# Optimization experiments

Measured on AMD Instinct MI355X. Metric: run time of the kernel, lower is better.

The kernel has to match this reference:

```python
import jax, jax.numpy as jnp
import numpy as np

B, S, H, D = 2, 2048, 16, 64
HID = H * D


def setup_inputs() -> dict:
    key = jax.random.key(0)
    ks = jax.random.split(key, 9)
    s = 1.0 / np.sqrt(HID).astype(np.float32)
    return {
        "hidden_states": jax.random.normal(ks[0], (B, S, HID), dtype=jnp.float32),
        "W_q": jax.random.normal(ks[1], (HID, HID), dtype=jnp.float32) * s,
        "W_k": jax.random.normal(ks[2], (HID, HID), dtype=jnp.float32) * s,
        "W_v": jax.random.normal(ks[3], (HID, HID), dtype=jnp.float32) * s,
        "W_o": jax.random.normal(ks[4], (HID, HID), dtype=jnp.float32) * s,
        "B_q": jax.random.normal(ks[5], (HID,), dtype=jnp.float32) * 0.02,
        "B_k": jax.random.normal(ks[6], (HID,), dtype=jnp.float32) * 0.02,
        "B_v": jax.random.normal(ks[7], (HID,), dtype=jnp.float32) * 0.02,
        "B_o": jax.random.normal(ks[8], (HID,), dtype=jnp.float32) * 0.02,
    }


def _split_heads(x):
    # (B, S, H*D) -> (B, H, S, D)
    b, s, _ = x.shape
    return x.reshape(b, s, H, D).transpose(0, 2, 1, 3)


def reference(hidden_states, W_q, W_k, W_v, W_o, B_q, B_k, B_v, B_o):
    q = _split_heads(hidden_states @ W_q + B_q)
    k = _split_heads(hidden_states @ W_k + B_k)
    v = _split_heads(hidden_states @ W_v + B_v)
    scale = 1.0 / jnp.sqrt(jnp.asarray(D, dtype=q.dtype))
    # (B, H, S, S) attention scores (no mask: original forward never applies it)
    scores = jnp.einsum("bhqd,bhkd->bhqk", q, k) * scale
    weights = jax.nn.softmax(scores, axis=-1)
    attended = jnp.einsum("bhqk,bhkd->bhqd", weights, v)
    # merge heads: (B, H, S, D) -> (B, S, H*D)
    merged = attended.transpose(0, 2, 1, 3).reshape(hidden_states.shape)
    return merged @ W_o + B_o
```

## Files before the change

kernel.cpp:

```cpp
#include <hip/hip_runtime.h>


typedef unsigned short u16;
typedef unsigned int u32;
typedef __attribute__((ext_vector_type(8))) __bf16 bf16x8;
typedef __attribute__((ext_vector_type(4))) float f32x4;
typedef __attribute__((ext_vector_type(16))) float f32x16;

#define MFMA16(a, b, c) __builtin_amdgcn_mfma_f32_16x16x32_bf16((a), (b), (c), 0, 0, 0)
#define MFMA32(a, b, c) __builtin_amdgcn_mfma_f32_32x32x16_bf16((a), (b), (c), 0, 0, 0)

#define GLOAD16(gp, lp)                                                        \
  __builtin_amdgcn_global_load_lds(                                           \
      (const __attribute__((address_space(1))) void*)(gp),                     \
      (__attribute__((address_space(3))) void*)(lp), 16, 0, 0)

static __device__ __forceinline__ u16 f2b(float f) {
  __bf16 b = (__bf16)f;
  return __builtin_bit_cast(u16, b);
}

static __device__ __forceinline__ u32 pk2(float lo, float hi) {
  return (u32)f2b(lo) | ((u32)f2b(hi) << 16);
}

static __device__ __forceinline__ float exp2_fast(float x) {
  float r;
  asm("v_exp_f32 %0, %1" : "=v"(r) : "v"(x));
  return r;
}

static __device__ __forceinline__ bf16x8 ld_glob16(const u16* p) {
  return __builtin_bit_cast(bf16x8, *(const uint4*)p);
}


__global__ void prep(const float* __restrict__ hidden,
                     const float* __restrict__ Wq, const float* __restrict__ Wk,
                     const float* __restrict__ Wv, const float* __restrict__ Wo,
                     const float* __restrict__ Bq, const float* __restrict__ Bk,
                     const float* __restrict__ Bv,
                     u16* __restrict__ hiddenB, u16* __restrict__ wqkvT,
                     u16* __restrict__ woT, float* __restrict__ biasQ) {
  __shared__ u16 tile[64][72];
  int z = blockIdx.z;
  int t = threadIdx.x;
  if (z < 4) {
    const float* W = (z == 0) ? Wq : (z == 1) ? Wk : (z == 2) ? Wv : Wo;
    int n0 = blockIdx.x * 64, k0 = blockIdx.y * 64;
#pragma unroll
    for (int i = 0; i < 16; ++i) {
      int idx = t + i * 256;
      int r = idx >> 6, c = idx & 63;
      tile[c][r] = f2b(W[(size_t)(k0 + r) * 1024 + n0 + c]);
    }
    __syncthreads();
    u16* dst = (z < 3) ? (wqkvT + (size_t)z * 1024 * 1024) : woT;
#pragma unroll
    for (int i = 0; i < 16; ++i) {
      int idx = t + i * 256;
      int r = idx >> 6, c = idx & 63;
      dst[(size_t)(n0 + r) * 1024 + k0 + c] = tile[r][c];
    }
  } else {
    int bid = blockIdx.y * 16 + blockIdx.x;
    int base = bid * 4096 + t;
#pragma unroll
    for (int i = 0; i < 16; ++i) {
      int idx = base + i * 256;
      float4 v = ((const float4*)hidden)[idx];
      ushort4 o;
      o.x = f2b(v.x); o.y = f2b(v.y); o.z = f2b(v.z); o.w = f2b(v.w);
      ((ushort4*)hiddenB)[idx] = o;
    }
    if (bid < 12) {
      int i = bid * 256 + t;
      float v = (i < 1024) ? Bq[i] : (i < 2048) ? Bk[i - 1024] : Bv[i - 2048];
      biasQ[i] = v;
    }
  }
}


template <bool OUT_BF16, bool QSCALE, bool VSPLIT>
__global__ __launch_bounds__(256) void gemm_bt(const u16* __restrict__ A,
                                               const u16* __restrict__ Bt,
                                               const float* __restrict__ bias,
                                               void* __restrict__ out,
                                               u16* __restrict__ vtb2,
                                               int K, int lda, int ldb, int ldo) {
  __shared__ __align__(16) char lds[49152];
  int nbx = gridDim.x;
  int f = blockIdx.x + nbx * blockIdx.y;
  int cpx = (nbx * gridDim.y) >> 3;
  int v = (f & 7) * cpx + (f >> 3);
  int m0 = (v % nbx) * 128, n0 = (v / nbx) * 128;
  int t = threadIdx.x, w = t >> 6, lane = t & 63, g = lane >> 4, ln = lane & 15;
  int wr = w >> 1, wc = w & 1;
  f32x4 acc[4][4] = {};
  int nkt = K >> 5;

#define STAGE_AB(bufoff, ktv)                                                  \
  {                                                                            \
    _Pragma("unroll")                                                          \
    for (int s = 0; s < 2; ++s) {                                              \
      int row = s * 64 + (t >> 2), c = t & 3, gg = c ^ ((row >> 1) & 3);       \
      GLOAD16(A + (size_t)(m0 + row) * lda + (ktv) * 32 + gg * 8,              \
              lds + (bufoff) + s * 4096 + w * 1024);                           \
      GLOAD16(Bt + (size_t)(n0 + row) * ldb + (ktv) * 32 + gg * 8,             \
              lds + (bufoff) + 8192 + s * 4096 + w * 1024);                    \
    }                                                                          \
  }

  STAGE_AB(0, 0);

  int bo = 0, so = 16384;
  for (int kt = 0; kt < nkt; ++kt) {
    if (kt < nkt - 1) {
      STAGE_AB(so, kt + 1);
      asm volatile("s_waitcnt vmcnt(4)" ::: "memory");
    } else {
      asm volatile("s_waitcnt vmcnt(0)" ::: "memory");
    }
    __builtin_amdgcn_s_barrier();
    asm volatile("" ::: "memory");

    const char* lA = lds + bo;
    const char* lB = lds + bo + 8192;
    bf16x8 af[4], bf_[4];
#pragma unroll
    for (int mi = 0; mi < 4; ++mi) {
      int row = wr * 64 + mi * 16 + ln;
      af[mi] = __builtin_bit_cast(
          bf16x8, *(const uint4*)(lA + row * 64 + ((g ^ ((row >> 1) & 3)) << 4)));
    }
#pragma unroll
    for (int ni = 0; ni < 4; ++ni) {
      int row = wc * 64 + ni * 16 + ln;
      bf_[ni] = __builtin_bit_cast(
          bf16x8, *(const uint4*)(lB + row * 64 + ((g ^ ((row >> 1) & 3)) << 4)));
    }
#pragma unroll
    for (int mi = 0; mi < 4; ++mi)
#pragma unroll
      for (int ni = 0; ni < 4; ++ni)
        acc[mi][ni] = MFMA16(af[mi], bf_[ni], acc[mi][ni]);

    int nx = so + 16384;
    if (nx == 49152) nx = 0;
    bo = so;
    so = nx;
  }
#undef STAGE_AB

#pragma unroll
  for (int mi = 0; mi < 4; ++mi) {
#pragma unroll
    for (int ni = 0; ni < 4; ++ni) {
      int n = n0 + wc * 64 + ni * 16 + ln;
      float bs = bias[n];
      float scale = QSCALE ? ((n < 1024) ? 0.18033688011f : 1.0f) : 1.0f;
      float vv[4];
#pragma unroll
      for (int r = 0; r < 4; ++r) vv[r] = (acc[mi][ni][r] + bs) * scale;
      int mbase = m0 + wr * 64 + mi * 16 + g * 4;
      if (VSPLIT && n >= 2048) {
        int bh = ((m0 >> 11) << 4) | ((n >> 6) & 15);
        int sloc = mbase & 2047;
        sloc = (sloc & ~15) | ((sloc & 4) << 1) | ((sloc & 8) >> 1);
        size_t vbase = (size_t)(bh * 64 + (n & 63)) * 2048 + sloc;
        *(uint2*)(vtb2 + vbase) = make_uint2(pk2(vv[0], vv[1]), pk2(vv[2], vv[3]));
      } else if (OUT_BF16) {
#pragma unroll
        for (int r = 0; r < 4; ++r)
          ((u16*)out)[(size_t)(mbase + r) * ldo + n] = f2b(vv[r]);
      } else {
#pragma unroll
        for (int r = 0; r < 4; ++r)
          ((float*)out)[(size_t)(mbase + r) * ldo + n] = vv[r];
      }
    }
  }
}

__global__ __launch_bounds__(256, 2) void attn(const u16* __restrict__ qkv,
                                               const u16* __restrict__ vt,
                                               u16* __restrict__ att) {
  __shared__ __align__(16) char lds[49152];

  int f = blockIdx.x + 16 * blockIdx.y;
  int v = (f & 7) * 64 + (f >> 3);
  int qt = v & 15, bh = v >> 4;
  int b = bh >> 4, h = bh & 15;

  int t = threadIdx.x, w = t >> 6, lane = t & 63;
  int col = lane & 31, hi = lane >> 5, a7 = lane & 7;

  int qrow = qt * 128 + w * 32 + col;
  const u16* qp = qkv + (size_t)(b * 2048 + qrow) * 3072 + h * 64;
  bf16x8 qf[4];
#pragma unroll
  for (int kst = 0; kst < 4; ++kst) qf[kst] = ld_glob16(qp + kst * 16 + hi * 8);

  int gg = (lane & 7) ^ (lane >> 3);
  const u16* kp0 = qkv + (size_t)(b * 2048 + 16 * w + (lane >> 3)) * 3072 + 1024 + h * 64 + gg * 8;
  const u16* vp0 = vt + (size_t)(bh * 64 + 16 * w + (lane >> 3)) * 2048 + gg * 8;

#define STAGE_KV(bufoff, itv)                                                  \
  {                                                                            \
    const u16* ka = kp0 + (size_t)(itv) * 196608;                              \
    const u16* va = vp0 + (size_t)(itv) * 64;                                  \
    GLOAD16(ka, lds + (bufoff) + 2048 * w);                                    \
    GLOAD16(ka + 24576, lds + (bufoff) + 2048 * w + 1024);                     \
    GLOAD16(va, lds + (bufoff) + 8192 + 2048 * w);                             \
    GLOAD16(va + 16384, lds + (bufoff) + 8192 + 2048 * w + 1024);              \
  }

  f32x16 O0 = {}, O1 = {};
  float lsum = 0.f;

  STAGE_KV(0, 0);

  int bo = 0, so = 16384;
  for (int it = 0; it < 32; ++it) {
    if (it < 31) {
      STAGE_KV(so, it + 1);
      asm volatile("s_waitcnt vmcnt(4)" ::: "memory");
    } else {
      asm volatile("s_waitcnt vmcnt(0)" ::: "memory");
    }
    __builtin_amdgcn_s_barrier();
    asm volatile("" ::: "memory");

    const char* lK = lds + bo;
    const char* lV = lds + bo + 8192;

    f32x16 s0 = {}, s1 = {};
    __builtin_amdgcn_s_setprio(1);
#pragma unroll
    for (int kst = 0; kst < 4; ++kst) {
      int slot = ((2 * kst + hi) ^ a7) << 4;
      bf16x8 k0 = *(const bf16x8*)(lK + col * 128 + slot);
      bf16x8 k1 = *(const bf16x8*)(lK + (32 + col) * 128 + slot);
      s0 = MFMA32(k0, qf[kst], s0);
      s1 = MFMA32(k1, qf[kst], s1);
    }
    __builtin_amdgcn_s_setprio(0);

    float a0 = 0.f, a1 = 0.f, a2 = 0.f, a3 = 0.f;
#pragma unroll
    for (int r = 0; r < 16; r += 4) {
      float p0 = exp2_fast(s0[r + 0]); s0[r + 0] = p0; a0 += p0;
      float p1 = exp2_fast(s0[r + 1]); s0[r + 1] = p1; a1 += p1;
      float p2 = exp2_fast(s0[r + 2]); s0[r + 2] = p2; a2 += p2;
      float p3 = exp2_fast(s0[r + 3]); s0[r + 3] = p3; a3 += p3;
    }
#pragma unroll
    for (int r = 0; r < 16; r += 4) {
      float p0 = exp2_fast(s1[r + 0]); s1[r + 0] = p0; a0 += p0;
      float p1 = exp2_fast(s1[r + 1]); s1[r + 1] = p1; a1 += p1;
      float p2 = exp2_fast(s1[r + 2]); s1[r + 2] = p2; a2 += p2;
      float p3 = exp2_fast(s1[r + 3]); s1[r + 3] = p3; a3 += p3;
    }
    lsum += (a0 + a1) + (a2 + a3);

    u32 cpk[2][8];
#pragma unroll
    for (int rp = 0; rp < 8; ++rp) {
      cpk[0][rp] = pk2(s0[2 * rp], s0[2 * rp + 1]);
      cpk[1][rp] = pk2(s1[2 * rp], s1[2 * rp + 1]);
    }

    __builtin_amdgcn_s_setprio(1);
#pragma unroll
    for (int ks = 0; ks < 4; ++ks) {
      const int tt = ks >> 1, base = (ks & 1) * 4;
      union { u32 u[4]; bf16x8 v8; } B;
      B.u[0] = cpk[tt][base + 0];
      B.u[1] = cpk[tt][base + 1];
      B.u[2] = cpk[tt][base + 2];
      B.u[3] = cpk[tt][base + 3];
      int slot = ((2 * ks + hi) ^ a7) << 4;
      bf16x8 v0 = *(const bf16x8*)(lV + col * 128 + slot);
      bf16x8 v1 = *(const bf16x8*)(lV + (32 + col) * 128 + slot);
      O0 = MFMA32(v0, B.v8, O0);
      O1 = MFMA32(v1, B.v8, O1);
    }
    __builtin_amdgcn_s_setprio(0);

    int nx = so + 16384;
    if (nx == 49152) nx = 0;
    bo = so;
    so = nx;
  }

  lsum += __shfl_xor(lsum, 32);

  float inv = 1.0f / lsum;
  char* tp = lds + w * 4096;
#pragma unroll
  for (int dt = 0; dt < 2; ++dt) {
#pragma unroll
    for (int g2 = 0; g2 < 4; ++g2) {
      float a0, a1, b0, b1;
      if (dt == 0) {
        a0 = O0[4 * g2 + 0]; a1 = O0[4 * g2 + 1];
        b0 = O0[4 * g2 + 2]; b1 = O0[4 * g2 + 3];
      } else {
        a0 = O1[4 * g2 + 0]; a1 = O1[4 * g2 + 1];
        b0 = O1[4 * g2 + 2]; b1 = O1[4 * g2 + 3];
      }
      u32 w0 = pk2(a0 * inv, a1 * inv);
      u32 w1 = pk2(b0 * inv, b1 * inv);
      int dq0 = 16 * dt + 4 * g2 + 2 * hi;
      int slot = dq0 ^ ((col & 7) << 2);
      *(uint2*)(tp + col * 128 + slot * 4) = make_uint2(w0, w1);
    }
  }
  asm volatile("s_waitcnt lgkmcnt(0)" ::: "memory");
  __builtin_amdgcn_sched_barrier(0);
  int q_r = lane >> 1, pr = lane & 1;
  size_t orow = (size_t)(b * 2048 + qt * 128 + w * 32 + q_r) * 1024 + h * 64;
#pragma unroll
  for (int j = 0; j < 4; ++j) {
    int dqb = 16 * pr + 4 * j;
    int slot = dqb ^ ((q_r & 7) << 2);
    uint4 val = *(const uint4*)(tp + q_r * 128 + slot * 4);
    *(uint4*)(att + orow + 2 * dqb) = val;
  }
#undef STAGE_KV
}


extern "C" void kernel_launch(void* const* d_in, const int* in_sizes, int n_in,
                              void* d_out, int out_size, void* d_ws, size_t ws_size,
                              hipStream_t stream) {
  const float* hidden = (const float*)d_in[0];
  const float* Wq = (const float*)d_in[1];
  const float* Wk = (const float*)d_in[2];
  const float* Wv = (const float*)d_in[3];
  const float* Wo = (const float*)d_in[4];
  const float* Bq = (const float*)d_in[5];
  const float* Bk = (const float*)d_in[6];
  const float* Bv = (const float*)d_in[7];
  const float* Bo = (const float*)d_in[8];

  char* ws = (char*)d_ws;
  u16* hiddenB = (u16*)(ws + 0);
  u16* wqkvT   = (u16*)(ws + 8388608);
  u16* woT     = (u16*)(ws + 14680064);
  float* biasQ = (float*)(ws + 16777216);
  u16* qkv     = (u16*)(ws + 16789504);
  u16* vtb     = (u16*)(ws + 41955328);
  u16* att     = hiddenB;

  prep<<<dim3(16, 16, 5), 256, 0, stream>>>(hidden, Wq, Wk, Wv, Wo, Bq, Bk, Bv,
                                            hiddenB, wqkvT, woT, biasQ);
  gemm_bt<true, true, true><<<dim3(32, 24), 256, 0, stream>>>(
      hiddenB, wqkvT, biasQ, qkv, vtb, 1024, 1024, 1024, 3072);
  attn<<<dim3(16, 32), 256, 0, stream>>>(qkv, vtb, att);
  gemm_bt<false, false, false><<<dim3(32, 8), 256, 0, stream>>>(
      att, woT, Bo, d_out, nullptr, 1024, 1024, 1024, 1024);
}
```

Before: 115.4 us.

## Deepen attention KV prefetch and use 64-row tiles for output projection

The attention kernel now keeps a four-buffer ring in LDS and prefetches K/V two iterations ahead, so it waits on older loads (vmcnt 8) and hides more global latency. The output-projection GEMM becomes its own kernel with 64x128 tiles, giving 512 blocks instead of 256 to fill more CUs. The QKV GEMM is specialised with compile-time sizes. Attention LDS grows to 64 KB per block, which may limit occupancy to the two blocks per CU that launch_bounds already asks for.

```diff
diff --git a/kernel.cpp b/kernel.cpp
--- a/kernel.cpp
+++ b/kernel.cpp
@@ -82,13 +82,12 @@
 }
 
 
-template <bool OUT_BF16, bool QSCALE, bool VSPLIT>
-__global__ __launch_bounds__(256) void gemm_bt(const u16* __restrict__ A,
-                                               const u16* __restrict__ Bt,
-                                               const float* __restrict__ bias,
-                                               void* __restrict__ out,
-                                               u16* __restrict__ vtb2,
-                                               int K, int lda, int ldb, int ldo) {
+__global__ __launch_bounds__(256) void gemm_qkv(const u16* __restrict__ A,
+                                                const u16* __restrict__ Bt,
+                                                const float* __restrict__ bias,
+                                                u16* __restrict__ out,
+                                                u16* __restrict__ vtb2) {
+  const int K = 1024, lda = 1024, ldb = 1024, ldo = 3072;
   __shared__ __align__(16) char lds[49152];
   int nbx = gridDim.x;
   int f = blockIdx.x + nbx * blockIdx.y;
@@ -159,26 +158,107 @@
     for (int ni = 0; ni < 4; ++ni) {
       int n = n0 + wc * 64 + ni * 16 + ln;
       float bs = bias[n];
-      float scale = QSCALE ? ((n < 1024) ? 0.18033688011f : 1.0f) : 1.0f;
+      float scale = (n < 1024) ? 0.18033688011f : 1.0f;
       float vv[4];
 #pragma unroll
       for (int r = 0; r < 4; ++r) vv[r] = (acc[mi][ni][r] + bs) * scale;
       int mbase = m0 + wr * 64 + mi * 16 + g * 4;
-      if (VSPLIT && n >= 2048) {
+      if (n >= 2048) {
         int bh = ((m0 >> 11) << 4) | ((n >> 6) & 15);
         int sloc = mbase & 2047;
         sloc = (sloc & ~15) | ((sloc & 4) << 1) | ((sloc & 8) >> 1);
         size_t vbase = (size_t)(bh * 64 + (n & 63)) * 2048 + sloc;
         *(uint2*)(vtb2 + vbase) = make_uint2(pk2(vv[0], vv[1]), pk2(vv[2], vv[3]));
-      } else if (OUT_BF16) {
+      } else {
 #pragma unroll
         for (int r = 0; r < 4; ++r)
-          ((u16*)out)[(size_t)(mbase + r) * ldo + n] = f2b(vv[r]);
-      } else {
-#pragma unroll
-        for (int r = 0; r < 4; ++r)
-          ((float*)out)[(size_t)(mbase + r) * ldo + n] = vv[r];
+          out[(size_t)(mbase + r) * ldo + n] = f2b(vv[r]);
       }
+    }
+  }
+}
+
+
+__global__ __launch_bounds__(256) void gemm_out(const u16* __restrict__ A,
+                                                const u16* __restrict__ Bt,
+                                                const float* __restrict__ bias,
+                                                float* __restrict__ out) {
+  const int K = 1024, lda = 1024, ldb = 1024, ldo = 1024;
+  __shared__ __align__(16) char lds[36864];
+  int nbx = gridDim.x;
+  int f = blockIdx.x + nbx * blockIdx.y;
+  int cpx = (nbx * gridDim.y) >> 3;
+  int v = (f & 7) * cpx + (f >> 3);
+  int m0 = (v % nbx) * 64, n0 = (v / nbx) * 128;
+  int t = threadIdx.x, w = t >> 6, lane = t & 63, g = lane >> 4, ln = lane & 15;
+  int wr = w >> 1, wc = w & 1;
+  f32x4 acc[2][4] = {};
+  int nkt = K >> 5;
+
+#define STAGE_AB64(bufoff, ktv)                                                \
+  {                                                                            \
+    int rowa = t >> 2, ca = t & 3, gga = ca ^ ((rowa >> 1) & 3);               \
+    GLOAD16(A + (size_t)(m0 + rowa) * lda + (ktv) * 32 + gga * 8,              \
+            lds + (bufoff) + w * 1024);                                        \
+    _Pragma("unroll")                                                          \
+    for (int s = 0; s < 2; ++s) {                                              \
+      int row = s * 64 + (t >> 2), c = t & 3, gg = c ^ ((row >> 1) & 3);       \
+      GLOAD16(Bt + (size_t)(n0 + row) * ldb + (ktv) * 32 + gg * 8,             \
+              lds + (bufoff) + 4096 + s * 4096 + w * 1024);                    \
+    }                                                                          \
+  }
+
+  STAGE_AB64(0, 0);
+
+  int bo = 0, so = 12288;
+  for (int kt = 0; kt < nkt; ++kt) {
+    if (kt < nkt - 1) {
+      STAGE_AB64(so, kt + 1);
+      asm volatile("s_waitcnt vmcnt(3)" ::: "memory");
+    } else {
+      asm volatile("s_waitcnt vmcnt(0)" ::: "memory");
+    }
+    __builtin_amdgcn_s_barrier();
+    asm volatile("" ::: "memory");
+
+    const char* lA = lds + bo;
+    const char* lB = lds + bo + 4096;
+    bf16x8 af[2], bf_[4];
+#pragma unroll
+    for (int mi = 0; mi < 2; ++mi) {
+      int row = wr * 32 + mi * 16 + ln;
+      af[mi] = __builtin_bit_cast(
+          bf16x8, *(const uint4*)(lA + row * 64 + ((g ^ ((row >> 1) & 3)) << 4)));
+    }
+#pragma unroll
+    for (int ni = 0; ni < 4; ++ni) {
+      int row = wc * 64 + ni * 16 + ln;
+      bf_[ni] = __builtin_bit_cast(
+          bf16x8, *(const uint4*)(lB + row * 64 + ((g ^ ((row >> 1) & 3)) << 4)));
+    }
+#pragma unroll
+    for (int mi = 0; mi < 2; ++mi)
+#pragma unroll
+      for (int ni = 0; ni < 4; ++ni)
+        acc[mi][ni] = MFMA16(af[mi], bf_[ni], acc[mi][ni]);
+
+    int nx = so + 12288;
+    if (nx == 36864) nx = 0;
+    bo = so;
+    so = nx;
+  }
+#undef STAGE_AB64
+
+#pragma unroll
+  for (int mi = 0; mi < 2; ++mi) {
+#pragma unroll
+    for (int ni = 0; ni < 4; ++ni) {
+      int n = n0 + wc * 64 + ni * 16 + ln;
+      float bs = bias[n];
+      int mbase = m0 + wr * 32 + mi * 16 + g * 4;
+#pragma unroll
+      for (int r = 0; r < 4; ++r)
+        out[(size_t)(mbase + r) * ldo + n] = acc[mi][ni][r] + bs;
     }
   }
 }
@@ -186,7 +266,7 @@
 __global__ __launch_bounds__(256, 2) void attn(const u16* __restrict__ qkv,
                                                const u16* __restrict__ vt,
                                                u16* __restrict__ att) {
-  __shared__ __align__(16) char lds[49152];
+  __shared__ __align__(16) char lds[65536];
 
   int f = blockIdx.x + 16 * blockIdx.y;
   int v = (f & 7) * 64 + (f >> 3);
@@ -220,11 +300,14 @@
   float lsum = 0.f;
 
   STAGE_KV(0, 0);
-
-  int bo = 0, so = 16384;
+  STAGE_KV(16384, 1);
+
   for (int it = 0; it < 32; ++it) {
-    if (it < 31) {
-      STAGE_KV(so, it + 1);
+    const int bufo = (it & 3) * 16384;
+    if (it < 30) {
+      STAGE_KV(((it + 2) & 3) * 16384, it + 2);
+      asm volatile("s_waitcnt vmcnt(8)" ::: "memory");
+    } else if (it == 30) {
       asm volatile("s_waitcnt vmcnt(4)" ::: "memory");
     } else {
       asm volatile("s_waitcnt vmcnt(0)" ::: "memory");
@@ -232,8 +315,8 @@
     __builtin_amdgcn_s_barrier();
     asm volatile("" ::: "memory");
 
-    const char* lK = lds + bo;
-    const char* lV = lds + bo + 8192;
+    const char* lK = lds + bufo;
+    const char* lV = lds + bufo + 8192;
 
     f32x16 s0 = {}, s1 = {};
     __builtin_amdgcn_s_setprio(1);
@@ -287,11 +370,6 @@
       O1 = MFMA32(v1, B.v8, O1);
     }
     __builtin_amdgcn_s_setprio(0);
-
-    int nx = so + 16384;
-    if (nx == 49152) nx = 0;
-    bo = so;
-    so = nx;
   }
 
   lsum += __shfl_xor(lsum, 32);
@@ -356,9 +434,7 @@
 
   prep<<<dim3(16, 16, 5), 256, 0, stream>>>(hidden, Wq, Wk, Wv, Wo, Bq, Bk, Bv,
                                             hiddenB, wqkvT, woT, biasQ);
-  gemm_bt<true, true, true><<<dim3(32, 24), 256, 0, stream>>>(
-      hiddenB, wqkvT, biasQ, qkv, vtb, 1024, 1024, 1024, 3072);
+  gemm_qkv<<<dim3(32, 24), 256, 0, stream>>>(hiddenB, wqkvT, biasQ, qkv, vtb);
   attn<<<dim3(16, 32), 256, 0, stream>>>(qkv, vtb, att);
-  gemm_bt<false, false, false><<<dim3(32, 8), 256, 0, stream>>>(
-      att, woT, Bo, d_out, nullptr, 1024, 1024, 1024, 1024);
-}
+  gemm_out<<<dim3(64, 8), 256, 0, stream>>>(att, woT, Bo, (float*)d_out);
+}
```

Result: slower. 119.0 us (+3.1%).
